# Kernel optimization log

Measured on AMD Instinct MI355X. Metric: run time of the kernel, lower is better.

## Reference

```python
import jax, jax.numpy as jnp
import numpy as np

INPUT_DIM, DIM_K, DIM_V = 1024, 512, 512

def setup_inputs() -> dict:
    key = jax.random.key(0)
    kx, kq, kk, kv = jax.random.split(key, 4)
    x = jax.random.normal(kx, (4, 4096, INPUT_DIM), dtype=jnp.float32)
    s = 1.0 / np.sqrt(INPUT_DIM)
    Wq = jax.random.normal(kq, (INPUT_DIM, DIM_K), dtype=jnp.float32) * s
    Wk = jax.random.normal(kk, (INPUT_DIM, DIM_K), dtype=jnp.float32) * s
    Wv = jax.random.normal(kv, (INPUT_DIM, DIM_V), dtype=jnp.float32) * s
    return {"x": x, "Wq": Wq, "Wk": Wk, "Wv": Wv}

def reference(x, Wq, Wk, Wv):
    # x: [b, n, d_in]; bias-free projections
    Q = jnp.einsum('bnd,dk->bnk', x, Wq)
    K = jnp.einsum('bnd,dk->bnk', x, Wk)
    V = jnp.einsum('bnd,dv->bnv', x, Wv)
    scale = 1.0 / np.sqrt(Wq.shape[1])
    scores = jnp.einsum('bqk,bnk->bqn', Q, K) * scale  # [b, n, n]
    atten = jax.nn.softmax(scores, axis=-1)
    return jnp.einsum('bqn,bnv->bqv', atten, V)
```

## Files before the change

### kernel.cpp

```cpp
#include <hip/hip_runtime.h>
#include <hip/hip_bf16.h>


typedef __attribute__((ext_vector_type(8))) short bf16x8;
typedef __attribute__((ext_vector_type(4))) float floatx4;

static __device__ __forceinline__ unsigned short f2bf(float f) {
    unsigned int u = __builtin_bit_cast(unsigned int, f);
    return (unsigned short)((u + 0x7fffu + ((u >> 16) & 1u)) >> 16);
}

static __device__ __forceinline__ void gl2lds16(const unsigned short* g, unsigned short* l) {
    __builtin_amdgcn_global_load_lds(
        (const __attribute__((address_space(1))) unsigned int*)g,
        (__attribute__((address_space(3))) unsigned int*)l, 16, 0, 0);
}

#define BAR() __asm__ volatile("s_barrier" ::: "memory")
#define WVMC4() __asm__ volatile("s_waitcnt vmcnt(4)" ::: "memory")
#define WVMC0() __asm__ volatile("s_waitcnt vmcnt(0)" ::: "memory")
#define WLGKM0() __asm__ volatile("s_waitcnt lgkmcnt(0)" ::: "memory")
#define WALL() __asm__ volatile("s_waitcnt vmcnt(0) lgkmcnt(0)" ::: "memory")

__global__ __launch_bounds__(256) void cvt_bf16(const float* __restrict__ X,
                                                unsigned short* __restrict__ Y, int n4) {
    int i = blockIdx.x * 256 + threadIdx.x;
    if (i < n4) {
        float4 v = reinterpret_cast<const float4*>(X)[i];
        ushort4 o;
        o.x = f2bf(v.x); o.y = f2bf(v.y); o.z = f2bf(v.z); o.w = f2bf(v.w);
        reinterpret_cast<ushort4*>(Y)[i] = o;
    }
}

__global__ __launch_bounds__(256) void transpose_w3(const float* __restrict__ Wq,
                                                    const float* __restrict__ Wk,
                                                    const float* __restrict__ Wv,
                                                    unsigned short* __restrict__ Wt) {
    __shared__ float tile[32][33];
    const float* W = (blockIdx.z == 0) ? Wq : (blockIdx.z == 1) ? Wk : Wv;
    const int off = blockIdx.z << 9;
    int n0 = blockIdx.x * 32;
    int k0 = blockIdx.y * 32;
    int tx = threadIdx.x & 31, ty = threadIdx.x >> 5;
    for (int i = 0; i < 32; i += 8)
        tile[ty + i][tx] = W[(size_t)(k0 + ty + i) * 512 + n0 + tx];
    __syncthreads();
    for (int i = 0; i < 32; i += 8)
        Wt[(size_t)(off + n0 + ty + i) * 1024 + k0 + tx] = f2bf(tile[tx][ty + i]);
}

__global__ __launch_bounds__(512, 2) void gemm_qkv(const unsigned short* __restrict__ A,
                                                   const unsigned short* __restrict__ Bt,
                                                   unsigned short* __restrict__ Qb,
                                                   unsigned short* __restrict__ Kfr,
                                                   unsigned short* __restrict__ Vfr) {
    __shared__ unsigned short AsU[3 * 16384];
    __shared__ unsigned short BsU[2 * 12288];

    const int L = blockIdx.x;
    const int i6 = L >> 3;
    const int mt = ((L & 7) << 3) | (i6 >> 3);
    const int nt = i6 & 7;
    const int m0 = mt << 8, n0 = nt * 192;
    const int tid = threadIdx.x;
    const int lane = tid & 63, wave = tid >> 6;
    const int wmi = wave >> 2, wni = wave & 3;
    const int quad = lane >> 4, l15 = lane & 15;

    const int srow = tid >> 3;
    const int sslot = (tid & 7) ^ ((tid >> 3) & 7);

    auto stageA = [&](int slot, int ktile, int c) {
        const unsigned short* src =
            A + (size_t)(m0 + c * 64 + srow) * 1024 + (ktile << 6) + sslot * 8;
        gl2lds16(src, AsU + slot * 16384 + c * 4096 + tid * 8);
    };
    auto stageB = [&](int slot, int ktile, int c) {
        const unsigned short* src =
            Bt + (size_t)(n0 + c * 64 + srow) * 1024 + (ktile << 6) + sslot * 8;
        gl2lds16(src, BsU + slot * 12288 + c * 4096 + tid * 8);
    };

    floatx4 acc[8][3] = {};

    for (int c = 0; c < 4; c++) stageA(0, 0, c);
    for (int c = 0; c < 3; c++) stageB(0, 0, c);
    for (int c = 0; c < 4; c++) stageA(1, 1, c);
    WVMC4();
    BAR();

    int cura = 0, curb = 0;
    for (int j = 0; j < 16; ++j) {
        const int nb = curb ^ 1;
        const int na = (cura >= 1) ? cura - 1 : cura + 2;
        const int ktB = (j + 1) & 15, ktA = (j + 2) & 15;
        const unsigned short* Ab = AsU + cura * 16384;
        const unsigned short* Bb = BsU + curb * 12288;

        bf16x8 af[4], bfr[3];
        const int arow = (wmi << 7) + l15;
        const int brow = wni * 48 + l15;
        const int sw = l15 & 7;

#pragma unroll
        for (int f = 0; f < 4; f++)
            af[f] = *reinterpret_cast<const bf16x8*>(Ab + (arow + f * 16) * 64 + (quad ^ sw) * 8);
#pragma unroll
        for (int f = 0; f < 3; f++)
            bfr[f] = *reinterpret_cast<const bf16x8*>(Bb + (brow + f * 16) * 64 + (quad ^ sw) * 8);
        stageB(nb, ktB, 0);
        stageB(nb, ktB, 1);
        BAR();
        __builtin_amdgcn_s_setprio(1);
#pragma unroll
        for (int f = 0; f < 4; f++)
#pragma unroll
            for (int g = 0; g < 3; g++)
                acc[f][g] = __builtin_amdgcn_mfma_f32_16x16x32_bf16(af[f], bfr[g], acc[f][g], 0, 0, 0);
        __builtin_amdgcn_s_setprio(0);
        BAR();

#pragma unroll
        for (int f = 0; f < 4; f++)
            af[f] = *reinterpret_cast<const bf16x8*>(Ab + (arow + (f + 4) * 16) * 64 + (quad ^ sw) * 8);
        stageB(nb, ktB, 2);
        stageA(na, ktA, 0);
        BAR();
        __builtin_amdgcn_s_setprio(1);
#pragma unroll
        for (int f = 0; f < 4; f++)
#pragma unroll
            for (int g = 0; g < 3; g++)
                acc[f + 4][g] = __builtin_amdgcn_mfma_f32_16x16x32_bf16(af[f], bfr[g], acc[f + 4][g], 0, 0, 0);
        __builtin_amdgcn_s_setprio(0);
        BAR();

#pragma unroll
        for (int f = 0; f < 4; f++)
            af[f] = *reinterpret_cast<const bf16x8*>(Ab + (arow + f * 16) * 64 + ((4 + quad) ^ sw) * 8);
#pragma unroll
        for (int f = 0; f < 3; f++)
            bfr[f] = *reinterpret_cast<const bf16x8*>(Bb + (brow + f * 16) * 64 + ((4 + quad) ^ sw) * 8);
        stageA(na, ktA, 1);
        stageA(na, ktA, 2);
        BAR();
        __builtin_amdgcn_s_setprio(1);
#pragma unroll
        for (int f = 0; f < 4; f++)
#pragma unroll
            for (int g = 0; g < 3; g++)
                acc[f][g] = __builtin_amdgcn_mfma_f32_16x16x32_bf16(af[f], bfr[g], acc[f][g], 0, 0, 0);
        __builtin_amdgcn_s_setprio(0);
        BAR();

#pragma unroll
        for (int f = 0; f < 4; f++)
            af[f] = *reinterpret_cast<const bf16x8*>(Ab + (arow + (f + 4) * 16) * 64 + ((4 + quad) ^ sw) * 8);
        stageA(na, ktA, 3);
        BAR();
        __builtin_amdgcn_s_setprio(1);
#pragma unroll
        for (int f = 0; f < 4; f++)
#pragma unroll
            for (int g = 0; g < 3; g++)
                acc[f + 4][g] = __builtin_amdgcn_mfma_f32_16x16x32_bf16(af[f], bfr[g], acc[f + 4][g], 0, 0, 0);
        __builtin_amdgcn_s_setprio(0);
        WVMC4();
        BAR();

        curb = nb;
        cura = (cura == 2) ? 0 : cura + 1;
    }
    WALL();

    const float qscale = 0.044194173824159216f;
#pragma unroll
    for (int fi = 0; fi < 8; fi++)
#pragma unroll
        for (int fj = 0; fj < 3; fj++)
#pragma unroll
            for (int r = 0; r < 4; r++) {
                int row = m0 + (wmi << 7) + fi * 16 + quad * 4 + r;
                int col = n0 + wni * 48 + fj * 16 + l15;
                if (col < 512) {
                    Qb[(size_t)row * 512 + col] = f2bf(acc[fi][fj][r] * qscale);
                } else if (col < 1024) {
                    int d = col - 512;
                    size_t base = ((size_t)((row >> 12) * 128 + ((row & 4095) >> 5))) << 14;
                    int off = ((d >> 5) * 2 + ((row >> 4) & 1)) * 512 +
                              (((d >> 3) & 3) * 16 + (row & 15)) * 8 + (d & 7);
                    Kfr[base + off] = f2bf(acc[fi][fj][r]);
                } else {
                    int d = col - 1024;
                    size_t base = ((size_t)((row >> 12) * 128 + ((row & 4095) >> 5))) << 14;
                    int off = (d >> 4) * 512 +
                              (((row & 31) >> 3) * 16 + (d & 15)) * 8 + (row & 7);
                    Vfr[base + off] = f2bf(acc[fi][fj][r]);
                }
            }
}

__global__ __launch_bounds__(512, 2) void attn(const unsigned short* __restrict__ Qg,
                                               const unsigned short* __restrict__ Kf,
                                               const unsigned short* __restrict__ Vf,
                                               float* __restrict__ O0,
                                               float* __restrict__ O1,
                                               float* __restrict__ lpart) {
    __shared__ unsigned short Kb[16384];
    __shared__ unsigned short Vb[3][16384];
    __shared__ unsigned short Ps[2][8][512];

    const int L = blockIdx.x;
    const int b = L & 3;
    const int h = (L >> 2) & 1;
    const int q0 = (L >> 3) * 128;
    const int tid = threadIdx.x;
    const int lane = tid & 63, wave = tid >> 6;
    const int quad = lane >> 4, l15 = lane & 15;
    const int qh = wave >> 2, dq = wave & 3;

    const unsigned short* KfB = Kf + ((size_t)b << 21);
    const unsigned short* VfB = Vf + ((size_t)b << 21);
    float* Od = (h == 0) ? O0 : O1;

    bf16x8 qf[16];
    {
        const unsigned short* qrow =
            Qg + (size_t)(b * 4096 + q0 + wave * 16 + l15) * 512 + quad * 8;
#pragma unroll
        for (int ks = 0; ks < 16; ks++)
            qf[ks] = *reinterpret_cast<const bf16x8*>(qrow + ks * 32);
    }
    WALL();

    floatx4 o[4][8];
#pragma unroll
    for (int g = 0; g < 4; g++)
#pragma unroll
        for (int n2 = 0; n2 < 8; n2++) o[g][n2] = floatx4{0.f, 0.f, 0.f, 0.f};
    float lp = 0.f;

    const int kt0 = h * 64;
    {
        const unsigned short* gK = KfB + ((size_t)kt0 << 14);
#pragma unroll
        for (int i = 0; i < 4; i++)
            gl2lds16(gK + (i * 512 + tid) * 8, &Kb[(i * 512 + tid) * 8]);
    }

    int vs = 0;
    for (int it = 0; it < 64; it++) {
        {
            const unsigned short* gV = VfB + ((size_t)(kt0 + it) << 14);
#pragma unroll
            for (int i = 0; i < 4; i++)
                gl2lds16(gV + (i * 512 + tid) * 8, &Vb[vs][(i * 512 + tid) * 8]);
        }
        WVMC4();
        BAR();

        const unsigned short* Kc = &Kb[0];
        floatx4 s00 = {0.f,0.f,0.f,0.f}, s01 = {0.f,0.f,0.f,0.f};
        floatx4 s10 = {0.f,0.f,0.f,0.f}, s11 = {0.f,0.f,0.f,0.f};
        __builtin_amdgcn_s_setprio(1);
#pragma unroll
        for (int ks = 0; ks < 16; ks += 2) {
            bf16x8 k0a = *reinterpret_cast<const bf16x8*>(Kc + (2 * ks + 0) * 512 + lane * 8);
            bf16x8 k1a = *reinterpret_cast<const bf16x8*>(Kc + (2 * ks + 1) * 512 + lane * 8);
            bf16x8 k0b = *reinterpret_cast<const bf16x8*>(Kc + (2 * ks + 2) * 512 + lane * 8);
            bf16x8 k1b = *reinterpret_cast<const bf16x8*>(Kc + (2 * ks + 3) * 512 + lane * 8);
            s00 = __builtin_amdgcn_mfma_f32_16x16x32_bf16(k0a, qf[ks], s00, 0, 0, 0);
            s10 = __builtin_amdgcn_mfma_f32_16x16x32_bf16(k1a, qf[ks], s10, 0, 0, 0);
            s01 = __builtin_amdgcn_mfma_f32_16x16x32_bf16(k0b, qf[ks + 1], s01, 0, 0, 0);
            s11 = __builtin_amdgcn_mfma_f32_16x16x32_bf16(k1b, qf[ks + 1], s11, 0, 0, 0);
        }
        __builtin_amdgcn_s_setprio(0);
        floatx4 s0v = s00 + s01, s1v = s10 + s11;

        {
            float p0[4], p1[4];
#pragma unroll
            for (int r = 0; r < 4; r++) {
                p0[r] = __expf(s0v[r] - 16.0f);
                p1[r] = __expf(s1v[r] - 16.0f);
                lp += p0[r] + p1[r];
            }
            unsigned int a0, a1, b0, b1;
            asm("v_cvt_pk_bf16_f32 %0, %1, %2" : "=v"(a0) : "v"(p0[0]), "v"(p0[1]));
            asm("v_cvt_pk_bf16_f32 %0, %1, %2" : "=v"(a1) : "v"(p0[2]), "v"(p0[3]));
            asm("v_cvt_pk_bf16_f32 %0, %1, %2" : "=v"(b0) : "v"(p1[0]), "v"(p1[1]));
            asm("v_cvt_pk_bf16_f32 %0, %1, %2" : "=v"(b1) : "v"(p1[2]), "v"(p1[3]));
            unsigned short* Pw = &Ps[it & 1][wave][0];
            const int wo = (quad >> 1) * 128 + l15 * 8 + (quad & 1) * 4;
            *reinterpret_cast<uint2*>(Pw + wo)       = uint2{a0, a1};
            *reinterpret_cast<uint2*>(Pw + wo + 256) = uint2{b0, b1};
        }
        WLGKM0();
        WVMC0();
        BAR();

        {
            const unsigned short* gK = KfB + ((size_t)(kt0 + ((it + 1) & 63)) << 14);
#pragma unroll
            for (int i = 0; i < 4; i++)
                gl2lds16(gK + (i * 512 + tid) * 8, &Kb[(i * 512 + tid) * 8]);
        }

        const unsigned short* Vc = &Vb[vs][0];
        bf16x8 vfr[8];
#pragma unroll
        for (int n2 = 0; n2 < 8; n2++)
            vfr[n2] = *reinterpret_cast<const bf16x8*>(Vc + (dq * 8 + n2) * 512 + lane * 8);
        __builtin_amdgcn_s_setprio(1);
#pragma unroll
        for (int g = 0; g < 4; g++) {
            bf16x8 pf = *reinterpret_cast<const bf16x8*>(&Ps[it & 1][qh * 4 + g][0] + lane * 8);
#pragma unroll
            for (int n2 = 0; n2 < 8; n2++)
                o[g][n2] = __builtin_amdgcn_mfma_f32_16x16x32_bf16(pf, vfr[n2], o[g][n2], 0, 0, 0);
        }
        __builtin_amdgcn_s_setprio(0);

        vs = (vs == 2) ? 0 : vs + 1;
    }
    WALL();

    lp += __shfl_xor(lp, 16);
    lp += __shfl_xor(lp, 32);
    if (quad == 0)
        lpart[h * 16384 + b * 4096 + q0 + wave * 16 + l15] = lp;

#pragma unroll
    for (int g = 0; g < 4; g++)
#pragma unroll
        for (int r = 0; r < 4; r++) {
            size_t rowoff = (size_t)(b * 4096 + q0 + qh * 64 + g * 16 + quad * 4 + r) * 512
                            + dq * 128 + l15;
#pragma unroll
            for (int n2 = 0; n2 < 8; n2++)
                Od[rowoff + n2 * 16] = o[g][n2][r];
        }
}

__global__ __launch_bounds__(256) void combine(float* __restrict__ Out,
                                               const float* __restrict__ O1,
                                               const float* __restrict__ lpart) {
    int i = blockIdx.x * 256 + threadIdx.x;
    int row = i >> 7;
    float inv = 1.0f / (lpart[row] + lpart[16384 + row]);
    float4 a = reinterpret_cast<const float4*>(Out)[i];
    float4 c = reinterpret_cast<const float4*>(O1)[i];
    float4 r;
    r.x = (a.x + c.x) * inv;
    r.y = (a.y + c.y) * inv;
    r.z = (a.z + c.z) * inv;
    r.w = (a.w + c.w) * inv;
    reinterpret_cast<float4*>(Out)[i] = r;
}

extern "C" void kernel_launch(void* const* d_in, const int* in_sizes, int n_in,
                              void* d_out, int out_size, void* d_ws, size_t ws_size,
                              hipStream_t stream) {
    const float* x  = (const float*)d_in[0];
    const float* Wq = (const float*)d_in[1];
    const float* Wk = (const float*)d_in[2];
    const float* Wv = (const float*)d_in[3];

    char* ws = (char*)d_ws;
    unsigned short* Wtall = (unsigned short*)(ws);
    unsigned short* Qb  = (unsigned short*)(ws + (3u << 20));
    unsigned short* Kfr = (unsigned short*)(ws + (19u << 20));
    unsigned short* Vfr = (unsigned short*)(ws + (35u << 20));
    unsigned short* xb  = (unsigned short*)(ws + (51u << 20));
    float* O1    = (float*)(ws + (51u << 20));
    float* lpart = (float*)(ws + (83u << 20));

    dim3 tb(256);
    cvt_bf16<<<dim3(16384), tb, 0, stream>>>(x, xb, 16384 * 1024 / 4);
    transpose_w3<<<dim3(16, 32, 3), tb, 0, stream>>>(Wq, Wk, Wv, Wtall);
    gemm_qkv<<<dim3(512), dim3(512), 0, stream>>>(xb, Wtall, Qb, Kfr, Vfr);
    attn<<<dim3(256), dim3(512), 0, stream>>>(Qb, Kfr, Vfr, (float*)d_out, O1, lpart);
    combine<<<dim3(8192), tb, 0, stream>>>((float*)d_out, O1, lpart);
}
```

Baseline: 339.4 us.

## Software-pipeline attention loop so QK of next tile overlaps PV of current

Restructures the attention main loop into a software pipeline. Each iteration now runs the QK^T and exp phase for tile it+1 together with the PV phase for tile it, so there is one barrier per iteration instead of two. K is double-buffered and V goes from three buffers to two, with a prologue and an epilogue added. The PV inner loop is reordered to load one V fragment at a time, which lowers register pressure but gives MFMA and exp work more room to interleave. The risk is extra live registers from overlapping the phases, which could hurt occupancy at the 512-thread launch bound of 2.

```diff
diff --git a/kernel.cpp b/kernel.cpp
--- a/kernel.cpp
+++ b/kernel.cpp
@@ -207,8 +207,8 @@
                                                float* __restrict__ O0,
                                                float* __restrict__ O1,
                                                float* __restrict__ lpart) {
-    __shared__ unsigned short Kb[16384];
-    __shared__ unsigned short Vb[3][16384];
+    __shared__ unsigned short Kr[2][16384];
+    __shared__ unsigned short Vb[2][16384];
     __shared__ unsigned short Ps[2][8][512];
 
     const int L = blockIdx.x;
@@ -242,25 +242,21 @@
     float lp = 0.f;
 
     const int kt0 = h * 64;
-    {
-        const unsigned short* gK = KfB + ((size_t)kt0 << 14);
+
+    auto stageK = [&](int j, int slot) {
+        const unsigned short* gK = KfB + ((size_t)(kt0 + (j & 63)) << 14);
 #pragma unroll
         for (int i = 0; i < 4; i++)
-            gl2lds16(gK + (i * 512 + tid) * 8, &Kb[(i * 512 + tid) * 8]);
-    }
-
-    int vs = 0;
-    for (int it = 0; it < 64; it++) {
-        {
-            const unsigned short* gV = VfB + ((size_t)(kt0 + it) << 14);
-#pragma unroll
-            for (int i = 0; i < 4; i++)
-                gl2lds16(gV + (i * 512 + tid) * 8, &Vb[vs][(i * 512 + tid) * 8]);
-        }
-        WVMC4();
-        BAR();
-
-        const unsigned short* Kc = &Kb[0];
+            gl2lds16(gK + (i * 512 + tid) * 8, &Kr[slot][(i * 512 + tid) * 8]);
+    };
+    auto stageV = [&](int j, int slot) {
+        const unsigned short* gV = VfB + ((size_t)(kt0 + (j & 63)) << 14);
+#pragma unroll
+        for (int i = 0; i < 4; i++)
+            gl2lds16(gV + (i * 512 + tid) * 8, &Vb[slot][(i * 512 + tid) * 8]);
+    };
+
+    auto qk_phase = [&](const unsigned short* Kc, floatx4& s0v, floatx4& s1v) {
         floatx4 s00 = {0.f,0.f,0.f,0.f}, s01 = {0.f,0.f,0.f,0.f};
         floatx4 s10 = {0.f,0.f,0.f,0.f}, s11 = {0.f,0.f,0.f,0.f};
         __builtin_amdgcn_s_setprio(1);
@@ -276,54 +272,72 @@
             s11 = __builtin_amdgcn_mfma_f32_16x16x32_bf16(k1b, qf[ks + 1], s11, 0, 0, 0);
         }
         __builtin_amdgcn_s_setprio(0);
-        floatx4 s0v = s00 + s01, s1v = s10 + s11;
-
-        {
-            float p0[4], p1[4];
-#pragma unroll
-            for (int r = 0; r < 4; r++) {
-                p0[r] = __expf(s0v[r] - 16.0f);
-                p1[r] = __expf(s1v[r] - 16.0f);
-                lp += p0[r] + p1[r];
-            }
-            unsigned int a0, a1, b0, b1;
-            asm("v_cvt_pk_bf16_f32 %0, %1, %2" : "=v"(a0) : "v"(p0[0]), "v"(p0[1]));
-            asm("v_cvt_pk_bf16_f32 %0, %1, %2" : "=v"(a1) : "v"(p0[2]), "v"(p0[3]));
-            asm("v_cvt_pk_bf16_f32 %0, %1, %2" : "=v"(b0) : "v"(p1[0]), "v"(p1[1]));
-            asm("v_cvt_pk_bf16_f32 %0, %1, %2" : "=v"(b1) : "v"(p1[2]), "v"(p1[3]));
-            unsigned short* Pw = &Ps[it & 1][wave][0];
-            const int wo = (quad >> 1) * 128 + l15 * 8 + (quad & 1) * 4;
-            *reinterpret_cast<uint2*>(Pw + wo)       = uint2{a0, a1};
-            *reinterpret_cast<uint2*>(Pw + wo + 256) = uint2{b0, b1};
+        s0v = s00 + s01;
+        s1v = s10 + s11;
+    };
+
+    auto sm_phase = [&](int slot, floatx4 s0v, floatx4 s1v) {
+        float p0[4], p1[4];
+#pragma unroll
+        for (int r = 0; r < 4; r++) {
+            p0[r] = __expf(s0v[r] - 16.0f);
+            p1[r] = __expf(s1v[r] - 16.0f);
+            lp += p0[r] + p1[r];
         }
+        unsigned int a0, a1, b0, b1;
+        asm("v_cvt_pk_bf16_f32 %0, %1, %2" : "=v"(a0) : "v"(p0[0]), "v"(p0[1]));
+        asm("v_cvt_pk_bf16_f32 %0, %1, %2" : "=v"(a1) : "v"(p0[2]), "v"(p0[3]));
+        asm("v_cvt_pk_bf16_f32 %0, %1, %2" : "=v"(b0) : "v"(p1[0]), "v"(p1[1]));
+        asm("v_cvt_pk_bf16_f32 %0, %1, %2" : "=v"(b1) : "v"(p1[2]), "v"(p1[3]));
+        unsigned short* Pw = &Ps[slot][wave][0];
+        const int wo = (quad >> 1) * 128 + l15 * 8 + (quad & 1) * 4;
+        *reinterpret_cast<uint2*>(Pw + wo)       = uint2{a0, a1};
+        *reinterpret_cast<uint2*>(Pw + wo + 256) = uint2{b0, b1};
+    };
+
+    auto pv_phase = [&](int slot) {
+        const unsigned short* Vc = &Vb[slot][0];
+        bf16x8 pf[4];
+#pragma unroll
+        for (int g = 0; g < 4; g++)
+            pf[g] = *reinterpret_cast<const bf16x8*>(&Ps[slot][qh * 4 + g][0] + lane * 8);
+        __builtin_amdgcn_s_setprio(1);
+#pragma unroll
+        for (int n2 = 0; n2 < 8; n2++) {
+            bf16x8 vfr = *reinterpret_cast<const bf16x8*>(Vc + (dq * 8 + n2) * 512 + lane * 8);
+#pragma unroll
+            for (int g = 0; g < 4; g++)
+                o[g][n2] = __builtin_amdgcn_mfma_f32_16x16x32_bf16(pf[g], vfr, o[g][n2], 0, 0, 0);
+        }
+        __builtin_amdgcn_s_setprio(0);
+    };
+
+    stageV(0, 0);
+    stageK(0, 0);
+    stageK(1, 1);
+    WVMC4();
+    BAR();
+    {
+        floatx4 s0v, s1v;
+        qk_phase(&Kr[0][0], s0v, s1v);
+        sm_phase(0, s0v, s1v);
+    }
+    WLGKM0();
+    WVMC0();
+    BAR();
+
+    for (int it = 0; it < 63; it++) {
+        stageV(it + 1, (it + 1) & 1);
+        stageK(it + 2, it & 1);
+        floatx4 s0v, s1v;
+        qk_phase(&Kr[(it + 1) & 1][0], s0v, s1v);
+        sm_phase((it + 1) & 1, s0v, s1v);
+        pv_phase(it & 1);
         WLGKM0();
         WVMC0();
         BAR();
-
-        {
-            const unsigned short* gK = KfB + ((size_t)(kt0 + ((it + 1) & 63)) << 14);
-#pragma unroll
-            for (int i = 0; i < 4; i++)
-                gl2lds16(gK + (i * 512 + tid) * 8, &Kb[(i * 512 + tid) * 8]);
-        }
-
-        const unsigned short* Vc = &Vb[vs][0];
-        bf16x8 vfr[8];
-#pragma unroll
-        for (int n2 = 0; n2 < 8; n2++)
-            vfr[n2] = *reinterpret_cast<const bf16x8*>(Vc + (dq * 8 + n2) * 512 + lane * 8);
-        __builtin_amdgcn_s_setprio(1);
-#pragma unroll
-        for (int g = 0; g < 4; g++) {
-            bf16x8 pf = *reinterpret_cast<const bf16x8*>(&Ps[it & 1][qh * 4 + g][0] + lane * 8);
-#pragma unroll
-            for (int n2 = 0; n2 < 8; n2++)
-                o[g][n2] = __builtin_amdgcn_mfma_f32_16x16x32_bf16(pf, vfr[n2], o[g][n2], 0, 0, 0);
-        }
-        __builtin_amdgcn_s_setprio(0);
-
-        vs = (vs == 2) ? 0 : vs + 1;
-    }
+    }
+    pv_phase(1);
     WALL();
 
     lp += __shfl_xor(lp, 16);
```

Result: no change. 338.3 us (-0.3%).
